# Kernel optimization log

Hardware: AMD Instinct MI355X
Metric: run time of the kernel (lower is better)

## Reference

```python
import jax, jax.numpy as jnp
import numpy as np

N_NODES, N_EDGES, D_IN, D_OUT = 40000, 640000, 128, 128


def setup_inputs() -> dict:
    key = jax.random.key(0)
    k0, k1, k2, k3, k4 = jax.random.split(key, 5)
    x = jax.random.normal(k0, (N_NODES, D_IN), dtype=jnp.float32)
    src = jax.random.randint(k1, (N_EDGES,), 0, N_NODES)
    dst = jax.random.randint(k2, (N_EDGES,), 0, N_NODES)
    edge_weight = jax.random.uniform(k3, (N_EDGES,), dtype=jnp.float32)
    # GraphConv learned parameters (Glorot-ish init) and bias
    W = jax.random.normal(k4, (D_IN, D_OUT), dtype=jnp.float32) * (1.0 / np.sqrt(D_IN))
    b = jnp.zeros((D_OUT,), dtype=jnp.float32)
    return {"x": x, "src": src, "dst": dst, "edge_weight": edge_weight, "W": W, "b": b}


def reference(x, src, dst, edge_weight, W, b):
    N = x.shape[0]
    # EdgeWeightNorm(norm='right') on all-ones edge weights: w_e = 1 / in_degree(dst_e)
    deg = jax.ops.segment_sum(jnp.ones_like(edge_weight), dst, num_segments=N)  # [N]
    inv_deg = jnp.where(deg > 0, 1.0 / deg, 0.0)  # allow_zero_in_degree
    w = inv_deg[dst] * edge_weight  # norm_weight *= self.edge_weight  [E]
    # GraphConv norm='none' with edge_weight: h[v] = sum_{e:(u->v)} w_e * x[u]
    msg = x[src] * w[:, None]  # [E, D_IN]
    h = jax.ops.segment_sum(msg, dst, num_segments=N)  # [N, D_IN]
    return h @ W + b  # [N, D_OUT]
```

## Files before the change

### kernel.cpp

```cpp
#include <hip/hip_runtime.h>

#define N_NODES 40000
#define N_EDGES 640000
#define D 128
#define NB 157
#define GEMM_ROWS 32


__global__ __launch_bounds__(256) void init_kernel(int* __restrict__ deg,
                                                   int* __restrict__ cursor) {
    int i = blockIdx.x * 256 + threadIdx.x;
    if (i < N_NODES) { deg[i] = 0; cursor[i] = 0; }
}

__global__ __launch_bounds__(256) void degree_kernel(const int* __restrict__ dst,
                                                     int* __restrict__ deg) {
    int e = blockIdx.x * 256 + threadIdx.x;
    if (e < N_EDGES) atomicAdd(&deg[dst[e]], 1);
}

__global__ __launch_bounds__(256) void reduce_kernel(const int* __restrict__ deg,
                                                     int* __restrict__ bsum) {
    __shared__ int s[256];
    int t = threadIdx.x;
    int idx = blockIdx.x * 256 + t;
    s[t] = (idx < N_NODES) ? deg[idx] : 0;
    __syncthreads();
#pragma unroll
    for (int off = 128; off > 0; off >>= 1) {
        if (t < off) s[t] += s[t + off];
        __syncthreads();
    }
    if (t == 0) bsum[blockIdx.x] = s[0];
}

__global__ __launch_bounds__(256) void offs_kernel(const int* __restrict__ deg,
                                                   const int* __restrict__ bsum,
                                                   int* __restrict__ offs,
                                                   float* __restrict__ invdeg) {
    __shared__ int s[256];
    __shared__ int base_s;
    int t = threadIdx.x;

    int v = (t < blockIdx.x && t < NB) ? bsum[t] : 0;
    s[t] = v;
    __syncthreads();
#pragma unroll
    for (int off = 128; off > 0; off >>= 1) {
        if (t < off) s[t] += s[t + off];
        __syncthreads();
    }
    if (t == 0) base_s = s[0];
    __syncthreads();
    int base = base_s;
    __syncthreads();

    int idx = blockIdx.x * 256 + t;
    int d = (idx < N_NODES) ? deg[idx] : 0;
    s[t] = d;
    __syncthreads();
#pragma unroll
    for (int off = 1; off < 256; off <<= 1) {
        int u = (t >= off) ? s[t - off] : 0;
        __syncthreads();
        s[t] += u;
        __syncthreads();
    }
    int excl = s[t] - d + base;
    if (idx < N_NODES) {
        offs[idx] = excl;
        invdeg[idx] = (d > 0) ? (1.0f / (float)d) : 0.0f;
        if (idx == N_NODES - 1) offs[N_NODES] = excl + d;
    }
}

__global__ __launch_bounds__(256) void bucket_kernel(const int* __restrict__ src,
                                                     const int* __restrict__ dst,
                                                     const float* __restrict__ ew,
                                                     const int* __restrict__ offs,
                                                     int* __restrict__ cursor,
                                                     int2* __restrict__ pairs) {
    int e = blockIdx.x * 256 + threadIdx.x;
    if (e >= N_EDGES) return;
    int d = dst[e];
    int pos = offs[d] + atomicAdd(&cursor[d], 1);
    pairs[pos] = make_int2(src[e], __float_as_int(ew[e]));
}

__global__ __launch_bounds__(256) void gemm_xw_kernel(const float* __restrict__ x,
                                                      const float* __restrict__ W,
                                                      float* __restrict__ y) {
    __shared__ float Ws[D * D];
    __shared__ float xs[GEMM_ROWS * D];
    const int tid = threadIdx.x;
    const int rowbase = blockIdx.x * GEMM_ROWS;

    float4* Ws4 = reinterpret_cast<float4*>(Ws);
    const float4* W4 = reinterpret_cast<const float4*>(W);
#pragma unroll
    for (int i = 0; i < 16; ++i)
        Ws4[tid + i * 256] = W4[tid + i * 256];

    float4* xs4 = reinterpret_cast<float4*>(xs);
    const float4* x4 = reinterpret_cast<const float4*>(x) + rowbase * (D / 4);
#pragma unroll
    for (int i = 0; i < GEMM_ROWS * (D / 4) / 256; ++i)
        xs4[tid + i * 256] = x4[tid + i * 256];
    __syncthreads();

    const int lane = tid & 31;
    const int rp   = tid >> 5;
    const float* xr0 = xs + (rp * 4 + 0) * D;
    const float* xr1 = xs + (rp * 4 + 1) * D;
    const float* xr2 = xs + (rp * 4 + 2) * D;
    const float* xr3 = xs + (rp * 4 + 3) * D;

    float4 a0 = {0.f,0.f,0.f,0.f}, a1 = a0, a2 = a0, a3 = a0;
#pragma unroll 4
    for (int k = 0; k < D; ++k) {
        float4 wv = Ws4[k * (D / 4) + lane];
        float x0 = xr0[k], x1 = xr1[k], x2 = xr2[k], x3 = xr3[k];
        a0.x += x0*wv.x; a0.y += x0*wv.y; a0.z += x0*wv.z; a0.w += x0*wv.w;
        a1.x += x1*wv.x; a1.y += x1*wv.y; a1.z += x1*wv.z; a1.w += x1*wv.w;
        a2.x += x2*wv.x; a2.y += x2*wv.y; a2.z += x2*wv.z; a2.w += x2*wv.w;
        a3.x += x3*wv.x; a3.y += x3*wv.y; a3.z += x3*wv.z; a3.w += x3*wv.w;
    }

    float4* y4 = reinterpret_cast<float4*>(y);
    int r0 = rowbase + rp * 4;
    y4[(r0 + 0) * (D / 4) + lane] = a0;
    y4[(r0 + 1) * (D / 4) + lane] = a1;
    y4[(r0 + 2) * (D / 4) + lane] = a2;
    y4[(r0 + 3) * (D / 4) + lane] = a3;
}

__global__ __launch_bounds__(256) void gather_kernel(const int* __restrict__ offs,
                                                     const int2* __restrict__ pairs,
                                                     const float* __restrict__ invdeg,
                                                     const float* __restrict__ y,
                                                     const float* __restrict__ b,
                                                     float* __restrict__ out) {
    int gid = blockIdx.x * 256 + threadIdx.x;
    int v    = gid >> 5;
    int part = gid & 31;
    if (v >= N_NODES) return;
    int beg = offs[v];
    int end = offs[v + 1];
    const float4* y4 = reinterpret_cast<const float4*>(y);
    float4 acc = {0.f, 0.f, 0.f, 0.f};
    for (int base = beg; base < end; base += 32) {
        int n = end - base; if (n > 32) n = 32;
        int2 pe = make_int2(0, 0);
        if (part < n) pe = pairs[base + part];
        for (int j = 0; j < n; ++j) {
            int   s = __shfl(pe.x, j, 32);
            float w = __int_as_float(__shfl(pe.y, j, 32));
            float4 t = y4[s * (D / 4) + part];
            acc.x += w * t.x; acc.y += w * t.y; acc.z += w * t.z; acc.w += w * t.w;
        }
    }
    float idv = invdeg[v];
    float4 bv = reinterpret_cast<const float4*>(b)[part];
    acc.x = acc.x * idv + bv.x;
    acc.y = acc.y * idv + bv.y;
    acc.z = acc.z * idv + bv.z;
    acc.w = acc.w * idv + bv.w;
    reinterpret_cast<float4*>(out)[v * (D / 4) + part] = acc;
}

extern "C" void kernel_launch(void* const* d_in, const int* in_sizes, int n_in,
                              void* d_out, int out_size, void* d_ws, size_t ws_size,
                              hipStream_t stream) {
    const float* x   = (const float*)d_in[0];
    const int*   src = (const int*)d_in[1];
    const int*   dst = (const int*)d_in[2];
    const float* ew  = (const float*)d_in[3];
    const float* W   = (const float*)d_in[4];
    const float* b   = (const float*)d_in[5];
    float* out = (float*)d_out;

    char* ws = (char*)d_ws;
    float* y      = (float*)ws;                       ws += (size_t)N_NODES * D * 4;
    int*   deg    = (int*)ws;                         ws += (size_t)N_NODES * 4;
    int*   cursor = (int*)ws;                         ws += (size_t)N_NODES * 4;
    float* invdeg = (float*)ws;                       ws += (size_t)N_NODES * 4;
    int*   offs   = (int*)ws;                         ws += (size_t)(N_NODES + 16) * 4;
    int*   bsum   = (int*)ws;                         ws += (size_t)((NB + 19) & ~3) * 4;
    int2*  pairs  = (int2*)ws;

    init_kernel<<<(N_NODES + 255) / 256, 256, 0, stream>>>(deg, cursor);
    degree_kernel<<<(N_EDGES + 255) / 256, 256, 0, stream>>>(dst, deg);
    reduce_kernel<<<NB, 256, 0, stream>>>(deg, bsum);
    offs_kernel<<<NB, 256, 0, stream>>>(deg, bsum, offs, invdeg);
    gemm_xw_kernel<<<N_NODES / GEMM_ROWS, 256, 0, stream>>>(x, W, y);
    bucket_kernel<<<(N_EDGES + 255) / 256, 256, 0, stream>>>(src, dst, ew,
                                                             offs, cursor, pairs);
    {
        long long total = (long long)N_NODES * 32;
        gather_kernel<<<(int)((total + 255) / 256), 256, 0, stream>>>(offs, pairs, invdeg, y, b, out);
    }
}
```

Baseline: 212.1 us.

## Reuse degree counter as bucket cursor, unroll gather by four with nontemporal memory ops

Drops the separate cursor array and init kernel. The bucket pass now decrements the degree counters with atomicSub to get slot positions, and deg is zeroed with hipMemsetAsync. The gather loop is unrolled by four with independent accumulators so more row loads of y are in flight at once. Pair loads and output stores use nontemporal hints, and bucket_kernel now runs before the GEMM. The changes cut one launch, the cursor traffic and the per-edge load latency chain, at the cost of more registers and a different floating-point summation order.

```diff
diff --git a/kernel.cpp b/kernel.cpp
--- a/kernel.cpp
+++ b/kernel.cpp
@@ -5,13 +5,10 @@
 #define D 128
 #define NB 157
 #define GEMM_ROWS 32
-
-
-__global__ __launch_bounds__(256) void init_kernel(int* __restrict__ deg,
-                                                   int* __restrict__ cursor) {
-    int i = blockIdx.x * 256 + threadIdx.x;
-    if (i < N_NODES) { deg[i] = 0; cursor[i] = 0; }
-}
+#define EDGE_BLOCKS ((N_EDGES + 255) / 256)
+
+typedef float f32x4 __attribute__((ext_vector_type(4)));
+
 
 __global__ __launch_bounds__(256) void degree_kernel(const int* __restrict__ dst,
                                                      int* __restrict__ deg) {
@@ -78,13 +75,16 @@
                                                      const int* __restrict__ dst,
                                                      const float* __restrict__ ew,
                                                      const int* __restrict__ offs,
-                                                     int* __restrict__ cursor,
-                                                     int2* __restrict__ pairs) {
+                                                     int* __restrict__ deg,
+                                                     long long* __restrict__ pairs) {
     int e = blockIdx.x * 256 + threadIdx.x;
     if (e >= N_EDGES) return;
     int d = dst[e];
-    int pos = offs[d] + atomicAdd(&cursor[d], 1);
-    pairs[pos] = make_int2(src[e], __float_as_int(ew[e]));
+    int c = atomicSub(&deg[d], 1);
+    int pos = offs[d] + c - 1;
+    unsigned long long packed = (unsigned long long)(unsigned int)src[e]
+                              | ((unsigned long long)__float_as_uint(ew[e]) << 32);
+    __builtin_nontemporal_store((long long)packed, &pairs[pos]);
 }
 
 __global__ __launch_bounds__(256) void gemm_xw_kernel(const float* __restrict__ x,
@@ -135,7 +135,7 @@
 }
 
 __global__ __launch_bounds__(256) void gather_kernel(const int* __restrict__ offs,
-                                                     const int2* __restrict__ pairs,
+                                                     const long long* __restrict__ pairs,
                                                      const float* __restrict__ invdeg,
                                                      const float* __restrict__ y,
                                                      const float* __restrict__ b,
@@ -147,25 +147,45 @@
     int beg = offs[v];
     int end = offs[v + 1];
     const float4* y4 = reinterpret_cast<const float4*>(y);
-    float4 acc = {0.f, 0.f, 0.f, 0.f};
+    float4 acc0 = {0.f,0.f,0.f,0.f}, acc1 = acc0, acc2 = acc0, acc3 = acc0;
     for (int base = beg; base < end; base += 32) {
         int n = end - base; if (n > 32) n = 32;
-        int2 pe = make_int2(0, 0);
-        if (part < n) pe = pairs[base + part];
-        for (int j = 0; j < n; ++j) {
-            int   s = __shfl(pe.x, j, 32);
-            float w = __int_as_float(__shfl(pe.y, j, 32));
+        long long pv = 0;
+        if (part < n) pv = __builtin_nontemporal_load(&pairs[base + part]);
+        int pex = (int)(unsigned int)((unsigned long long)pv & 0xffffffffull);
+        int pey = (int)(unsigned int)((unsigned long long)pv >> 32);
+        int j = 0;
+        for (; j + 4 <= n; j += 4) {
+            int   s0 = __shfl(pex, j + 0, 32), s1 = __shfl(pex, j + 1, 32);
+            int   s2 = __shfl(pex, j + 2, 32), s3 = __shfl(pex, j + 3, 32);
+            float w0 = __int_as_float(__shfl(pey, j + 0, 32));
+            float w1 = __int_as_float(__shfl(pey, j + 1, 32));
+            float w2 = __int_as_float(__shfl(pey, j + 2, 32));
+            float w3 = __int_as_float(__shfl(pey, j + 3, 32));
+            float4 t0 = y4[s0 * (D / 4) + part];
+            float4 t1 = y4[s1 * (D / 4) + part];
+            float4 t2 = y4[s2 * (D / 4) + part];
+            float4 t3 = y4[s3 * (D / 4) + part];
+            acc0.x += w0*t0.x; acc0.y += w0*t0.y; acc0.z += w0*t0.z; acc0.w += w0*t0.w;
+            acc1.x += w1*t1.x; acc1.y += w1*t1.y; acc1.z += w1*t1.z; acc1.w += w1*t1.w;
+            acc2.x += w2*t2.x; acc2.y += w2*t2.y; acc2.z += w2*t2.z; acc2.w += w2*t2.w;
+            acc3.x += w3*t3.x; acc3.y += w3*t3.y; acc3.z += w3*t3.z; acc3.w += w3*t3.w;
+        }
+        for (; j < n; ++j) {
+            int   s = __shfl(pex, j, 32);
+            float w = __int_as_float(__shfl(pey, j, 32));
             float4 t = y4[s * (D / 4) + part];
-            acc.x += w * t.x; acc.y += w * t.y; acc.z += w * t.z; acc.w += w * t.w;
+            acc0.x += w*t.x; acc0.y += w*t.y; acc0.z += w*t.z; acc0.w += w*t.w;
         }
     }
     float idv = invdeg[v];
     float4 bv = reinterpret_cast<const float4*>(b)[part];
-    acc.x = acc.x * idv + bv.x;
-    acc.y = acc.y * idv + bv.y;
-    acc.z = acc.z * idv + bv.z;
-    acc.w = acc.w * idv + bv.w;
-    reinterpret_cast<float4*>(out)[v * (D / 4) + part] = acc;
+    f32x4 r;
+    r.x = (acc0.x + acc1.x + acc2.x + acc3.x) * idv + bv.x;
+    r.y = (acc0.y + acc1.y + acc2.y + acc3.y) * idv + bv.y;
+    r.z = (acc0.z + acc1.z + acc2.z + acc3.z) * idv + bv.z;
+    r.w = (acc0.w + acc1.w + acc2.w + acc3.w) * idv + bv.w;
+    __builtin_nontemporal_store(r, reinterpret_cast<f32x4*>(out) + v * (D / 4) + part);
 }
 
 extern "C" void kernel_launch(void* const* d_in, const int* in_sizes, int n_in,
@@ -182,21 +202,21 @@
     char* ws = (char*)d_ws;
     float* y      = (float*)ws;                       ws += (size_t)N_NODES * D * 4;
     int*   deg    = (int*)ws;                         ws += (size_t)N_NODES * 4;
-    int*   cursor = (int*)ws;                         ws += (size_t)N_NODES * 4;
     float* invdeg = (float*)ws;                       ws += (size_t)N_NODES * 4;
     int*   offs   = (int*)ws;                         ws += (size_t)(N_NODES + 16) * 4;
     int*   bsum   = (int*)ws;                         ws += (size_t)((NB + 19) & ~3) * 4;
-    int2*  pairs  = (int2*)ws;
-
-    init_kernel<<<(N_NODES + 255) / 256, 256, 0, stream>>>(deg, cursor);
-    degree_kernel<<<(N_EDGES + 255) / 256, 256, 0, stream>>>(dst, deg);
+    long long* pairs = (long long*)ws;
+
+    hipMemsetAsync(deg, 0, (size_t)N_NODES * 4, stream);
+
+    degree_kernel<<<EDGE_BLOCKS, 256, 0, stream>>>(dst, deg);
     reduce_kernel<<<NB, 256, 0, stream>>>(deg, bsum);
     offs_kernel<<<NB, 256, 0, stream>>>(deg, bsum, offs, invdeg);
+    bucket_kernel<<<EDGE_BLOCKS, 256, 0, stream>>>(src, dst, ew, offs, deg, pairs);
     gemm_xw_kernel<<<N_NODES / GEMM_ROWS, 256, 0, stream>>>(x, W, y);
-    bucket_kernel<<<(N_EDGES + 255) / 256, 256, 0, stream>>>(src, dst, ew,
-                                                             offs, cursor, pairs);
     {
         long long total = (long long)N_NODES * 32;
-        gather_kernel<<<(int)((total + 255) / 256), 256, 0, stream>>>(offs, pairs, invdeg, y, b, out);
-    }
-}
+        gather_kernel<<<(int)((total + 255) / 256), 256, 0, stream>>>(
+            offs, pairs, invdeg, y, b, out);
+    }
+}
```

Result: slower. 219.2 us (+3.3%).

## Replace per-node CSR build with coarse bucket sort and LDS-atomic aggregation

Applied to the files above, without the earlier changes.

Swaps the per-node counting sort (degree, two-level scan, per-edge global atomic scatter) for a coarse sort into 1024 buckets of 40 nodes. Per-block LDS histograms cut global atomics, and packed 64-bit edge records carry the source, the local node index and the weight. The aggregation kernel then accumulates each bucket's rows in shared memory with LDS float atomics, which replaces one warp per node. This trades fewer launches and less global atomic traffic for LDS atomic contention, only 64 blocks in the scatter phases, and a 16-bit src field that relies on node ids below 65536.

```diff
diff --git a/kernel.cpp b/kernel.cpp
--- a/kernel.cpp
+++ b/kernel.cpp
@@ -3,88 +3,86 @@
 #define N_NODES 40000
 #define N_EDGES 640000
 #define D 128
-#define NB 157
 #define GEMM_ROWS 32
-
-
-__global__ __launch_bounds__(256) void init_kernel(int* __restrict__ deg,
-                                                   int* __restrict__ cursor) {
-    int i = blockIdx.x * 256 + threadIdx.x;
-    if (i < N_NODES) { deg[i] = 0; cursor[i] = 0; }
-}
-
-__global__ __launch_bounds__(256) void degree_kernel(const int* __restrict__ dst,
-                                                     int* __restrict__ deg) {
-    int e = blockIdx.x * 256 + threadIdx.x;
-    if (e < N_EDGES) atomicAdd(&deg[dst[e]], 1);
-}
-
-__global__ __launch_bounds__(256) void reduce_kernel(const int* __restrict__ deg,
-                                                     int* __restrict__ bsum) {
-    __shared__ int s[256];
+#define NBUCK 1024
+#define NPB   40
+#define HB    64
+#define EPHB  (N_EDGES / HB)
+
+typedef float f32x4 __attribute__((ext_vector_type(4)));
+typedef unsigned long long u64;
+
+
+__global__ __launch_bounds__(256) void histdeg_kernel(const int* __restrict__ dst,
+                                                      int* __restrict__ deg,
+                                                      int* __restrict__ ccnt) {
+    __shared__ int hist[NBUCK];
+    const int tid = threadIdx.x;
+    for (int i = tid; i < NBUCK; i += 256) hist[i] = 0;
+    __syncthreads();
+    const int base = blockIdx.x * EPHB;
+    for (int i = tid; i < EPHB; i += 256) {
+        int d = dst[base + i];
+        atomicAdd(&deg[d], 1);
+        atomicAdd(&hist[d / NPB], 1);
+    }
+    __syncthreads();
+    for (int i = tid; i < NBUCK; i += 256) {
+        int h = hist[i];
+        if (h) atomicAdd(&ccnt[i], h);
+    }
+}
+
+__global__ __launch_bounds__(1024) void scan_kernel(const int* __restrict__ ccnt,
+                                                    int* __restrict__ cbase,
+                                                    int* __restrict__ ccur) {
+    __shared__ int s[NBUCK];
     int t = threadIdx.x;
-    int idx = blockIdx.x * 256 + t;
-    s[t] = (idx < N_NODES) ? deg[idx] : 0;
+    int v = ccnt[t];
+    s[t] = v;
     __syncthreads();
 #pragma unroll
-    for (int off = 128; off > 0; off >>= 1) {
-        if (t < off) s[t] += s[t + off];
-        __syncthreads();
-    }
-    if (t == 0) bsum[blockIdx.x] = s[0];
-}
-
-__global__ __launch_bounds__(256) void offs_kernel(const int* __restrict__ deg,
-                                                   const int* __restrict__ bsum,
-                                                   int* __restrict__ offs,
-                                                   float* __restrict__ invdeg) {
-    __shared__ int s[256];
-    __shared__ int base_s;
-    int t = threadIdx.x;
-
-    int v = (t < blockIdx.x && t < NB) ? bsum[t] : 0;
-    s[t] = v;
-    __syncthreads();
-#pragma unroll
-    for (int off = 128; off > 0; off >>= 1) {
-        if (t < off) s[t] += s[t + off];
-        __syncthreads();
-    }
-    if (t == 0) base_s = s[0];
-    __syncthreads();
-    int base = base_s;
-    __syncthreads();
-
-    int idx = blockIdx.x * 256 + t;
-    int d = (idx < N_NODES) ? deg[idx] : 0;
-    s[t] = d;
-    __syncthreads();
-#pragma unroll
-    for (int off = 1; off < 256; off <<= 1) {
+    for (int off = 1; off < NBUCK; off <<= 1) {
         int u = (t >= off) ? s[t - off] : 0;
         __syncthreads();
         s[t] += u;
         __syncthreads();
     }
-    int excl = s[t] - d + base;
-    if (idx < N_NODES) {
-        offs[idx] = excl;
-        invdeg[idx] = (d > 0) ? (1.0f / (float)d) : 0.0f;
-        if (idx == N_NODES - 1) offs[N_NODES] = excl + d;
-    }
-}
-
-__global__ __launch_bounds__(256) void bucket_kernel(const int* __restrict__ src,
-                                                     const int* __restrict__ dst,
-                                                     const float* __restrict__ ew,
-                                                     const int* __restrict__ offs,
-                                                     int* __restrict__ cursor,
-                                                     int2* __restrict__ pairs) {
-    int e = blockIdx.x * 256 + threadIdx.x;
-    if (e >= N_EDGES) return;
-    int d = dst[e];
-    int pos = offs[d] + atomicAdd(&cursor[d], 1);
-    pairs[pos] = make_int2(src[e], __float_as_int(ew[e]));
+    int excl = s[t] - v;
+    cbase[t] = excl;
+    ccur[t]  = excl;
+    if (t == NBUCK - 1) cbase[NBUCK] = excl + v;
+}
+
+__global__ __launch_bounds__(256) void scatterA_kernel(const int* __restrict__ src,
+                                                       const int* __restrict__ dst,
+                                                       const float* __restrict__ ew,
+                                                       int* __restrict__ ccur,
+                                                       u64* __restrict__ pairs) {
+    __shared__ int hbase[NBUCK];
+    __shared__ int lcur[NBUCK];
+    const int tid = threadIdx.x;
+    for (int i = tid; i < NBUCK; i += 256) hbase[i] = 0;
+    __syncthreads();
+    const int base = blockIdx.x * EPHB;
+    for (int i = tid; i < EPHB; i += 256)
+        atomicAdd(&hbase[dst[base + i] / NPB], 1);
+    __syncthreads();
+    for (int i = tid; i < NBUCK; i += 256) {
+        int h = hbase[i];
+        hbase[i] = h ? atomicAdd(&ccur[i], h) : 0;
+        lcur[i] = 0;
+    }
+    __syncthreads();
+    for (int i = tid; i < EPHB; i += 256) {
+        int d = dst[base + i];
+        int bk = d / NPB;
+        int loc = d - bk * NPB;
+        int pos = hbase[bk] + atomicAdd(&lcur[bk], 1);
+        u64 pk = (u64)(unsigned int)(src[base + i] | (loc << 16))
+               | ((u64)__float_as_uint(ew[base + i]) << 32);
+        pairs[pos] = pk;
+    }
 }
 
 __global__ __launch_bounds__(256) void gemm_xw_kernel(const float* __restrict__ x,
@@ -134,38 +132,73 @@
     y4[(r0 + 3) * (D / 4) + lane] = a3;
 }
 
-__global__ __launch_bounds__(256) void gather_kernel(const int* __restrict__ offs,
-                                                     const int2* __restrict__ pairs,
-                                                     const float* __restrict__ invdeg,
-                                                     const float* __restrict__ y,
-                                                     const float* __restrict__ b,
-                                                     float* __restrict__ out) {
-    int gid = blockIdx.x * 256 + threadIdx.x;
-    int v    = gid >> 5;
-    int part = gid & 31;
-    if (v >= N_NODES) return;
-    int beg = offs[v];
-    int end = offs[v + 1];
-    const float4* y4 = reinterpret_cast<const float4*>(y);
-    float4 acc = {0.f, 0.f, 0.f, 0.f};
-    for (int base = beg; base < end; base += 32) {
-        int n = end - base; if (n > 32) n = 32;
-        int2 pe = make_int2(0, 0);
-        if (part < n) pe = pairs[base + part];
-        for (int j = 0; j < n; ++j) {
-            int   s = __shfl(pe.x, j, 32);
-            float w = __int_as_float(__shfl(pe.y, j, 32));
-            float4 t = y4[s * (D / 4) + part];
-            acc.x += w * t.x; acc.y += w * t.y; acc.z += w * t.z; acc.w += w * t.w;
+__global__ __launch_bounds__(256) void passB_kernel(const int* __restrict__ cbase,
+                                                    const u64* __restrict__ pairs,
+                                                    const int* __restrict__ deg,
+                                                    const float* __restrict__ y,
+                                                    const float* __restrict__ b,
+                                                    float* __restrict__ out) {
+    __shared__ float acc[NPB * D];
+    const int bkt = blockIdx.x;
+    const int node0 = bkt * NPB;
+    if (node0 >= N_NODES) return;
+    const int tid  = threadIdx.x;
+    const int part = tid & 31;
+    const int g    = tid >> 5;
+
+    for (int i = tid; i < NPB * D; i += 256) acc[i] = 0.f;
+    __syncthreads();
+
+    const int eb = cbase[bkt], ee = cbase[bkt + 1];
+    for (int e0 = eb + g * 2; e0 < ee; e0 += 16) {
+        u64 p0 = __builtin_nontemporal_load(&pairs[e0]);
+        int  has1 = (e0 + 1 < ee);
+        u64 p1 = has1 ? __builtin_nontemporal_load(&pairs[e0 + 1]) : 0;
+
+        int   s0 = (int)(p0 & 0xffffu);
+        int   l0 = (int)((p0 >> 16) & 0xffu);
+        float w0 = __uint_as_float((unsigned int)(p0 >> 32));
+        const float* yr0 = y + s0 * D + part;
+        float v00 = yr0[0], v01 = yr0[32], v02 = yr0[64], v03 = yr0[96];
+
+        int   s1 = (int)(p1 & 0xffffu);
+        int   l1 = (int)((p1 >> 16) & 0xffu);
+        float w1 = __uint_as_float((unsigned int)(p1 >> 32));
+        const float* yr1 = y + s1 * D + part;
+        float v10 = 0.f, v11 = 0.f, v12 = 0.f, v13 = 0.f;
+        if (has1) { v10 = yr1[0]; v11 = yr1[32]; v12 = yr1[64]; v13 = yr1[96]; }
+
+        float* a0 = acc + l0 * D + part;
+        atomicAdd(a0 +  0, w0 * v00);
+        atomicAdd(a0 + 32, w0 * v01);
+        atomicAdd(a0 + 64, w0 * v02);
+        atomicAdd(a0 + 96, w0 * v03);
+        if (has1) {
+            float* a1 = acc + l1 * D + part;
+            atomicAdd(a1 +  0, w1 * v10);
+            atomicAdd(a1 + 32, w1 * v11);
+            atomicAdd(a1 + 64, w1 * v12);
+            atomicAdd(a1 + 96, w1 * v13);
         }
     }
-    float idv = invdeg[v];
-    float4 bv = reinterpret_cast<const float4*>(b)[part];
-    acc.x = acc.x * idv + bv.x;
-    acc.y = acc.y * idv + bv.y;
-    acc.z = acc.z * idv + bv.z;
-    acc.w = acc.w * idv + bv.w;
-    reinterpret_cast<float4*>(out)[v * (D / 4) + part] = acc;
+    __syncthreads();
+
+    const float4* b4 = reinterpret_cast<const float4*>(b);
+    f32x4* out4 = reinterpret_cast<f32x4*>(out);
+    int nrows = N_NODES - node0; if (nrows > NPB) nrows = NPB;
+    for (int r = g; r < nrows; r += 8) {
+        int node = node0 + r;
+        int dg = deg[node];
+        float inv = (dg > 0) ? (1.0f / (float)dg) : 0.0f;
+        float4 bv = b4[part];
+        const float* ar = acc + r * D + part * 4;
+        f32x4 o;
+        o.x = ar[0] * inv + bv.x;
+        o.y = ar[1] * inv + bv.y;
+        o.z = ar[2] * inv + bv.z;
+        o.w = ar[3] * inv + bv.w;
+        __builtin_nontemporal_store(o, out4 + node * (D / 4) + part);
+    }
 }
 
 extern "C" void kernel_launch(void* const* d_in, const int* in_sizes, int n_in,
@@ -180,23 +213,18 @@
     float* out = (float*)d_out;
 
     char* ws = (char*)d_ws;
-    float* y      = (float*)ws;                       ws += (size_t)N_NODES * D * 4;
-    int*   deg    = (int*)ws;                         ws += (size_t)N_NODES * 4;
-    int*   cursor = (int*)ws;                         ws += (size_t)N_NODES * 4;
-    float* invdeg = (float*)ws;                       ws += (size_t)N_NODES * 4;
-    int*   offs   = (int*)ws;                         ws += (size_t)(N_NODES + 16) * 4;
-    int*   bsum   = (int*)ws;                         ws += (size_t)((NB + 19) & ~3) * 4;
-    int2*  pairs  = (int2*)ws;
-
-    init_kernel<<<(N_NODES + 255) / 256, 256, 0, stream>>>(deg, cursor);
-    degree_kernel<<<(N_EDGES + 255) / 256, 256, 0, stream>>>(dst, deg);
-    reduce_kernel<<<NB, 256, 0, stream>>>(deg, bsum);
-    offs_kernel<<<NB, 256, 0, stream>>>(deg, bsum, offs, invdeg);
+    float* y     = (float*)ws;                        ws += (size_t)N_NODES * D * 4;
+    int*   deg   = (int*)ws;                          ws += (size_t)N_NODES * 4;
+    int*   ccnt  = (int*)ws;                          ws += (size_t)NBUCK * 4;
+    int*   cbase = (int*)ws;                          ws += (size_t)(NBUCK + 4) * 4;
+    int*   ccur  = (int*)ws;                          ws += (size_t)NBUCK * 4;
+    u64*   pairs = (u64*)ws;
+
+    hipMemsetAsync(deg, 0, (size_t)(N_NODES + NBUCK) * 4, stream);
+
+    histdeg_kernel<<<HB, 256, 0, stream>>>(dst, deg, ccnt);
+    scan_kernel<<<1, NBUCK, 0, stream>>>(ccnt, cbase, ccur);
+    scatterA_kernel<<<HB, 256, 0, stream>>>(src, dst, ew, ccur, pairs);
     gemm_xw_kernel<<<N_NODES / GEMM_ROWS, 256, 0, stream>>>(x, W, y);
-    bucket_kernel<<<(N_EDGES + 255) / 256, 256, 0, stream>>>(src, dst, ew,
-                                                             offs, cursor, pairs);
-    {
-        long long total = (long long)N_NODES * 32;
-        gather_kernel<<<(int)((total + 255) / 256), 256, 0, stream>>>(offs, pairs, invdeg, y, b, out);
-    }
-}
+    passB_kernel<<<NBUCK, 256, 0, stream>>>(cbase, pairs, deg, y, b, out);
+}
```

New measurement: 601.9 us. 184% more time.
